# Kernel optimization log

Hardware: AMD Instinct MI355X
Metric: run time of the kernel (lower is better)

## Reference

```python
import jax, jax.numpy as jnp
import numpy as np

HID = 128  # args['hidden_size']


def preprocess_adj(A):
    # A: [B, N, N] -> D^{-1/2} (A + I) D^{-1/2}
    N = A.shape[1]
    A_hat = A + jnp.eye(N, dtype=A.dtype)
    d = jnp.sum(A_hat, axis=2)                     # [B, N]
    d_safe = jnp.where(d > 0, d, 1.0)
    d_inv = jnp.where(d > 0, d_safe ** -0.5, 0.0)  # inf -> 0, as in torch code
    return d_inv[:, :, None] * A_hat * d_inv[:, None, :]


def lstm(x, w_ih, w_hh, b_ih, b_hh):
    # x: [B, T, H]; PyTorch gate order i, f, g, o; zero init state
    B = x.shape[0]
    H = w_hh.shape[1]
    def step(carry, xt):
        h, c = carry
        z = xt @ w_ih.T + b_ih + h @ w_hh.T + b_hh
        i, f, g, o = jnp.split(z, 4, axis=-1)
        c = jax.nn.sigmoid(f) * c + jax.nn.sigmoid(i) * jnp.tanh(g)
        h = jax.nn.sigmoid(o) * jnp.tanh(c)
        return (h, c), h
    h0 = jnp.zeros((B, H), x.dtype)
    c0 = jnp.zeros((B, H), x.dtype)
    _, hs = jax.lax.scan(step, (h0, c0), jnp.swapaxes(x, 0, 1))
    return jnp.swapaxes(hs, 0, 1)  # [B, T, H]


def gcn_dynamic_forward(x, A_norm, conv_w, conv_b, w_ih, w_hh, b_ih, b_hh):
    # x: [B, N, HID] with N >= HID: take last HID rows as dynamic-filter input
    df_in = x[:, x.shape[1] - HID:, :]              # [B, HID, HID]
    dyn = jax.lax.conv_general_dilated(
        df_in, conv_w, window_strides=(1,), padding=[(1, 1)],
        dimension_numbers=('NCH', 'OIH', 'NCH')) + conv_b[None, :, None]
    lw = lstm(dyn, w_ih, w_hh, b_ih, b_hh)          # [B, HID, HID]
    agg = jnp.matmul(A_norm, x)                     # [B, N, HID]
    out = jax.nn.sigmoid(jnp.matmul(agg, lw))       # output activation (1-layer GCN)
    return out                                       # dropout is identity in eval


def setup_inputs() -> dict:
    key = jax.random.key(0)
    ks = jax.random.split(key, 8)
    B, N = 4, 4096
    node_embedding = jax.random.normal(ks[0], (B, N, HID), dtype=jnp.float32)
    # sparse symmetric-ish 0/1 adjacency, avg degree ~ N*0.01
    adjacency_matrix = (jax.random.uniform(ks[1], (B, N, N)) < 0.01).astype(jnp.float32)
    s = 0.05
    conv_w = jax.random.normal(ks[2], (HID, HID, 3), dtype=jnp.float32) * s
    conv_b = jax.random.normal(ks[3], (HID,), dtype=jnp.float32) * s
    w_ih = jax.random.normal(ks[4], (4 * HID, HID), dtype=jnp.float32) * s
    w_hh = jax.random.normal(ks[5], (4 * HID, HID), dtype=jnp.float32) * s
    b_ih = jax.random.normal(ks[6], (4 * HID,), dtype=jnp.float32) * s
    b_hh = jax.random.normal(ks[7], (4 * HID,), dtype=jnp.float32) * s
    return {"node_embedding": node_embedding, "adjacency_matrix": adjacency_matrix,
            "conv_w": conv_w, "conv_b": conv_b,
            "w_ih": w_ih, "w_hh": w_hh, "b_ih": b_ih, "b_hh": b_hh}


def reference(node_embedding, adjacency_matrix, conv_w, conv_b, w_ih, w_hh, b_ih, b_hh):
    A_norm = preprocess_adj(adjacency_matrix)
    return gcn_dynamic_forward(node_embedding, A_norm, conv_w, conv_b, w_ih, w_hh, b_ih, b_hh)
```

## Files before the change

kernel.cpp:

```cpp
#include <hip/hip_runtime.h>
#include <math.h>

#define N_NODES 4096
#define HIDN 128
#define MAXNZ 128

typedef float v4f __attribute__((ext_vector_type(4)));
typedef _Float16 h2 __attribute__((ext_vector_type(2)));
typedef _Float16 h8 __attribute__((ext_vector_type(8)));

__device__ __forceinline__ float fsig(float x) { return 1.0f / (1.0f + __expf(-x)); }
__device__ __forceinline__ float ftanh_(float x) { return 1.0f - 2.0f / (__expf(2.0f * x) + 1.0f); }

__global__ __launch_bounds__(512) void k_scan_conv(
        const float* __restrict__ A, float* __restrict__ d_inv,
        int* __restrict__ cnt, int* __restrict__ idx,
        const float* __restrict__ x, const float* __restrict__ conv_w,
        const float* __restrict__ conv_b, const float* __restrict__ w_ih,
        const float* __restrict__ b_ih, const float* __restrict__ b_hh,
        float* __restrict__ z4) {
    if (blockIdx.x < 2048) {
        const int wid = threadIdx.x >> 6;
        const int lane = threadIdx.x & 63;
        const int r = blockIdx.x * 8 + wid;
        const v4f* row = (const v4f*)(A + (size_t)r * N_NODES);
        __shared__ int sidx[8][MAXNZ];
        const unsigned long long below = (1ull << lane) - 1ull;
        int cbase = 0;
        v4f v[16];
        #pragma unroll
        for (int j = 0; j < 16; ++j)
            v[j] = row[j * 64 + lane];
#define PROC1(c, col)                                                         \
        {                                                                     \
            bool nz = ((c) != 0.0f);                                          \
            unsigned long long mm = __ballot(nz);                             \
            if (mm) {                                                         \
                if (nz) {                                                     \
                    int p_ = cbase + __popcll(mm & below);                    \
                    if (p_ < MAXNZ) sidx[wid][p_] = (col);                    \
                }                                                             \
                cbase += __popcll(mm);                                        \
            }                                                                 \
        }
        #pragma unroll
        for (int j = 0; j < 16; ++j) {
            int col0 = (j * 64 + lane) * 4;
            PROC1(v[j].x, col0 + 0);
            PROC1(v[j].y, col0 + 1);
            PROC1(v[j].z, col0 + 2);
            PROC1(v[j].w, col0 + 3);
        }
#undef PROC1
        int cnt_r = (cbase < MAXNZ) ? cbase : MAXNZ;
        for (int k = lane; k < cnt_r; k += 64)
            idx[r * MAXNZ + k] = sidx[wid][k];
        if (lane == 0) {
            cnt[r] = cnt_r;
            d_inv[r] = rsqrtf((float)(cbase + 1));
        }
    } else {
        const int cb = blockIdx.x - 2048;
        const int b = cb >> 5;
        const int t0 = (cb & 31) * 4;
        const int tsub = threadIdx.x >> 7;
        const int h = threadIdx.x & 127;
        const int t = t0 + tsub;
        __shared__ __align__(16) float dyn_lds[4][HIDN];
        const float* xb = x + ((size_t)b * N_NODES + (N_NODES - HIDN)) * HIDN;
        const float* w = conv_w + (size_t)t * HIDN * 3;
        float a0 = conv_b[t], a1 = 0.0f, a2 = 0.0f, a3 = 0.0f;
        #pragma unroll 4
        for (int i = 0; i < HIDN; i += 4) {
            const float* xr0 = xb + (size_t)i * HIDN;
            #pragma unroll
            for (int s = 0; s < 4; ++s) {
                const float* xr = xr0 + s * HIDN;
                float w0 = w[(i + s) * 3 + 0], w1 = w[(i + s) * 3 + 1], w2 = w[(i + s) * 3 + 2];
                float left  = (h > 0)   ? xr[h - 1] : 0.0f;
                float mid   = xr[h];
                float right = (h < 127) ? xr[h + 1] : 0.0f;
                if (s == 0)      a0 += left * w0 + mid * w1 + right * w2;
                else if (s == 1) a1 += left * w0 + mid * w1 + right * w2;
                else if (s == 2) a2 += left * w0 + mid * w1 + right * w2;
                else             a3 += left * w0 + mid * w1 + right * w2;
            }
        }
        dyn_lds[tsub][h] = (a0 + a1) + (a2 + a3);
        __syncthreads();
        const float4* dyn4 = (const float4*)dyn_lds[tsub];
        const int ch = t >> 4, si = t & 15;
        for (int qg = 0; qg < 4; ++qg) {
            int u = h + 128 * qg;
            const float4* wr = (const float4*)(w_ih + (size_t)u * HIDN);
            float za = b_ih[u] + b_hh[u];
            #pragma unroll
            for (int f4 = 0; f4 < 32; ++f4) {
                float4 wv = wr[f4];
                float4 dv = dyn4[f4];
                za += wv.x * dv.x + wv.y * dv.y + wv.z * dv.z + wv.w * dv.w;
            }
            z4[(((size_t)(b * 8 + ch) * 128 + h) * 4 + qg) * 16 + si] = za;
        }
    }
}

__global__ __launch_bounds__(512) void k_lstm_gather(
        const float* __restrict__ z4, const float* __restrict__ w_hh,
        float* __restrict__ lw,
        const float* __restrict__ x, const float* __restrict__ d_inv,
        const int* __restrict__ cnt, const int* __restrict__ idx,
        float* __restrict__ agg) {
    if (blockIdx.x < 4) {
        const int b = blockIdx.x;
        const int t = threadIdx.x;
        const int m = t >> 2;
        const int q = t & 3;
        __shared__ __align__(16) h2 hbuf[2][64];
        h2 w2[4][16];
        #pragma unroll
        for (int g = 0; g < 4; ++g) {
            const float4* wr = (const float4*)(w_hh + ((size_t)(g * HIDN + m)) * HIDN + q * 32);
            #pragma unroll
            for (int j4 = 0; j4 < 8; ++j4) {
                float4 wv = wr[j4];
                w2[g][2 * j4 + 0] = h2{(_Float16)wv.x, (_Float16)wv.y};
                w2[g][2 * j4 + 1] = h2{(_Float16)wv.z, (_Float16)wv.w};
            }
        }
        float c = 0.0f;
        if (t < 64) hbuf[0][t] = h2{(_Float16)0.0f, (_Float16)0.0f};
        __syncthreads();
        for (int ch = 0; ch < 8; ++ch) {
            const float4* zc = (const float4*)(z4 + ((((size_t)(b * 8 + ch) * 128 + m) * 4 + q) * 16));
            float4 zr0 = zc[0], zr1 = zc[1], zr2 = zc[2], zr3 = zc[3];
            float zs[16] = {zr0.x, zr0.y, zr0.z, zr0.w, zr1.x, zr1.y, zr1.z, zr1.w,
                            zr2.x, zr2.y, zr2.z, zr2.w, zr3.x, zr3.y, zr3.z, zr3.w};
            float hist[16];
            #pragma unroll
            for (int si = 0; si < 16; ++si) {
                const int s = ch * 16 + si;
                const h8* hq8 = ((const h8*)hbuf[s & 1]) + q * 4;
                h8 H0 = hq8[0], H1 = hq8[1], H2 = hq8[2], H3 = hq8[3];
                h2 hh[16];
                #pragma unroll
                for (int j = 0; j < 4; ++j) {
                    hh[j]      = ((const h2*)&H0)[j];
                    hh[4 + j]  = ((const h2*)&H1)[j];
                    hh[8 + j]  = ((const h2*)&H2)[j];
                    hh[12 + j] = ((const h2*)&H3)[j];
                }
                float zq = zs[si];
                float a0 = (q == 0) ? zq : 0.0f, b0 = 0.0f;
                float a1 = (q == 1) ? zq : 0.0f, b1 = 0.0f;
                float a2 = (q == 2) ? zq : 0.0f, b2 = 0.0f;
                float a3 = (q == 3) ? zq : 0.0f, b3 = 0.0f;
                #pragma unroll
                for (int j = 0; j < 8; ++j) {
                    a0 = __builtin_amdgcn_fdot2(w2[0][2 * j], hh[2 * j], a0, false);
                    b0 = __builtin_amdgcn_fdot2(w2[0][2 * j + 1], hh[2 * j + 1], b0, false);
                    a1 = __builtin_amdgcn_fdot2(w2[1][2 * j], hh[2 * j], a1, false);
                    b1 = __builtin_amdgcn_fdot2(w2[1][2 * j + 1], hh[2 * j + 1], b1, false);
                    a2 = __builtin_amdgcn_fdot2(w2[2][2 * j], hh[2 * j], a2, false);
                    b2 = __builtin_amdgcn_fdot2(w2[2][2 * j + 1], hh[2 * j + 1], b2, false);
                    a3 = __builtin_amdgcn_fdot2(w2[3][2 * j], hh[2 * j], a3, false);
                    b3 = __builtin_amdgcn_fdot2(w2[3][2 * j + 1], hh[2 * j + 1], b3, false);
                }
                float z0 = a0 + b0, z1 = a1 + b1, z2 = a2 + b2, z3 = a3 + b3;
                z0 += __shfl_xor(z0, 1); z0 += __shfl_xor(z0, 2);
                z1 += __shfl_xor(z1, 1); z1 += __shfl_xor(z1, 2);
                z2 += __shfl_xor(z2, 1); z2 += __shfl_xor(z2, 2);
                z3 += __shfl_xor(z3, 1); z3 += __shfl_xor(z3, 2);
                float ig = fsig(z0);
                float fg = fsig(z1);
                float gg = ftanh_(z2);
                float og = fsig(z3);
                c = fg * c + ig * gg;
                float hn = og * ftanh_(c);
                hist[si] = hn;
                if (q == 0) ((_Float16*)hbuf[(s + 1) & 1])[m] = (_Float16)hn;
                __syncthreads();
            }
            float* lwb = lw + ((size_t)b * HIDN + ch * 16) * HIDN + m;
            #pragma unroll
            for (int qq = 0; qq < 4; ++qq) {
                if (q == qq) {
                    #pragma unroll
                    for (int k = 0; k < 4; ++k)
                        lwb[(size_t)(qq * 4 + k) * HIDN] = hist[qq * 4 + k];
                }
            }
        }
    } else {
        const int gIdx = blockIdx.x - 4;
        const int b = (gIdx & 7) >> 1;
        const int o = ((gIdx >> 3) << 1) | (gIdx & 1);
        const int wid = threadIdx.x >> 6;
        const int lane = threadIdx.x & 63;
        __shared__ __align__(16) float dl[N_NODES];
        {
            const float4* dsrc = (const float4*)(d_inv + (b << 12));
            float4* ddst = (float4*)dl;
            ddst[threadIdx.x] = dsrc[threadIdx.x];
            ddst[threadIdx.x + 512] = dsrc[threadIdx.x + 512];
        }
        __syncthreads();
        const int i = o * 8 + wid;
        const int r = (b << 12) + i;
        const float2* xb = (const float2*)(x + (size_t)b * N_NODES * HIDN);
        const int* irow = idx + r * MAXNZ;
        const int n = cnt[r];
        float ax = 0.0f, ay = 0.0f;
        int k = 0;
        for (; k + 8 <= n; k += 8) {
            int4 j0 = *(const int4*)&irow[k];
            int4 j1 = *(const int4*)&irow[k + 4];
            float2 v0 = xb[(size_t)j0.x * 64 + lane];
            float2 v1 = xb[(size_t)j0.y * 64 + lane];
            float2 v2 = xb[(size_t)j0.z * 64 + lane];
            float2 v3 = xb[(size_t)j0.w * 64 + lane];
            float2 v4 = xb[(size_t)j1.x * 64 + lane];
            float2 v5 = xb[(size_t)j1.y * 64 + lane];
            float2 v6 = xb[(size_t)j1.z * 64 + lane];
            float2 v7 = xb[(size_t)j1.w * 64 + lane];
            float d0 = dl[j0.x], d1 = dl[j0.y], d2 = dl[j0.z], d3 = dl[j0.w];
            float d4 = dl[j1.x], d5 = dl[j1.y], d6 = dl[j1.z], d7 = dl[j1.w];
            ax += d0 * v0.x + d1 * v1.x + d2 * v2.x + d3 * v3.x
                + d4 * v4.x + d5 * v5.x + d6 * v6.x + d7 * v7.x;
            ay += d0 * v0.y + d1 * v1.y + d2 * v2.y + d3 * v3.y
                + d4 * v4.y + d5 * v5.y + d6 * v6.y + d7 * v7.y;
        }
        for (; k < n; ++k) {
            int j = irow[k];
            float dj = dl[j];
            float2 v = xb[(size_t)j * 64 + lane];
            ax += dj * v.x;
            ay += dj * v.y;
        }
        float di = dl[i];
        float2 vi = xb[(size_t)i * 64 + lane];
        float2 o2;
        o2.x = di * (ax + di * vi.x);
        o2.y = di * (ay + di * vi.y);
        ((float2*)(agg + (size_t)r * HIDN))[lane] = o2;
    }
}

__global__ __launch_bounds__(256) void k_outmm(
        const float* __restrict__ agg, const float* __restrict__ lw,
        float* __restrict__ out) {
    __shared__ __align__(16) float lw_lds[HIDN * HIDN];
    const int i0 = blockIdx.x * 64;
    const int b = i0 >> 12;
    const float4* lwg = (const float4*)(lw + (size_t)b * HIDN * HIDN);
    float4* lds4 = (float4*)lw_lds;
    for (int v = threadIdx.x; v < HIDN * HIDN / 4; v += 256) lds4[v] = lwg[v];
    __syncthreads();
    const int r0 = i0 + (threadIdx.x >> 3) * 2;
    const int u0 = (threadIdx.x & 7) * 16;
    const float4* a4 = (const float4*)agg;
    float4 acc[2][4];
    #pragma unroll
    for (int rr = 0; rr < 2; ++rr)
        #pragma unroll
        for (int cc = 0; cc < 4; ++cc) acc[rr][cc] = make_float4(0.f, 0.f, 0.f, 0.f);
    for (int f4 = 0; f4 < 32; ++f4) {
        float4 a0 = a4[(size_t)r0 * 32 + f4];
        float4 a1 = a4[(size_t)(r0 + 1) * 32 + f4];
        #pragma unroll
        for (int ff = 0; ff < 4; ++ff) {
            float af0 = (ff == 0) ? a0.x : (ff == 1) ? a0.y : (ff == 2) ? a0.z : a0.w;
            float af1 = (ff == 0) ? a1.x : (ff == 1) ? a1.y : (ff == 2) ? a1.z : a1.w;
            int f = f4 * 4 + ff;
            const float4* wrow = (const float4*)(lw_lds + f * HIDN + u0);
            #pragma unroll
            for (int cc = 0; cc < 4; ++cc) {
                float4 wv = wrow[cc];
                acc[0][cc].x += af0 * wv.x; acc[0][cc].y += af0 * wv.y;
                acc[0][cc].z += af0 * wv.z; acc[0][cc].w += af0 * wv.w;
                acc[1][cc].x += af1 * wv.x; acc[1][cc].y += af1 * wv.y;
                acc[1][cc].z += af1 * wv.z; acc[1][cc].w += af1 * wv.w;
            }
        }
    }
    #pragma unroll
    for (int rr = 0; rr < 2; ++rr) {
        #pragma unroll
        for (int cc = 0; cc < 4; ++cc) {
            float4 ov;
            ov.x = fsig(acc[rr][cc].x);
            ov.y = fsig(acc[rr][cc].y);
            ov.z = fsig(acc[rr][cc].z);
            ov.w = fsig(acc[rr][cc].w);
            *(float4*)(out + (size_t)(r0 + rr) * HIDN + u0 + cc * 4) = ov;
        }
    }
}

extern "C" void kernel_launch(void* const* d_in, const int* in_sizes, int n_in,
                              void* d_out, int out_size, void* d_ws, size_t ws_size,
                              hipStream_t stream) {
    const float* x      = (const float*)d_in[0];
    const float* A      = (const float*)d_in[1];
    const float* conv_w = (const float*)d_in[2];
    const float* conv_b = (const float*)d_in[3];
    const float* w_ih   = (const float*)d_in[4];
    const float* w_hh   = (const float*)d_in[5];
    const float* b_ih   = (const float*)d_in[6];
    const float* b_hh   = (const float*)d_in[7];
    float* out = (float*)d_out;

    char* ws = (char*)d_ws;
    float* d_inv = (float*)ws;
    int*   cnt   = (int*)(ws + 65536);
    int*   idx   = (int*)(ws + 131072);
    float* z4    = (float*)(ws + 131072 + 8388608);
    float* lw    = (float*)(ws + 131072 + 8388608 + 1048576);
    float* agg   = (float*)(ws + 131072 + 8388608 + 1048576 + 262144);

    hipLaunchKernelGGL(k_scan_conv, dim3(2176), dim3(512), 0, stream,
                       A, d_inv, cnt, idx,
                       x, conv_w, conv_b, w_ih, b_ih, b_hh, z4);
    hipLaunchKernelGGL(k_lstm_gather, dim3(2052), dim3(512), 0, stream,
                       z4, w_hh, lw, x, d_inv, cnt, idx, agg);
    hipLaunchKernelGGL(k_outmm, dim3(256), dim3(256), 0, stream, agg, lw, out);
}
```

Before: 562.5 us.

## Split fused scan/conv kernel and software-pipeline adjacency row scan

Splits the combined adjacency-scan and conv/input-projection kernel into two separate kernels. The conv kernel now has each thread compute one gate row across four timesteps, reusing each w_ih row for four dot products and writing the results as a float4. The scan kernel uses 256-thread blocks and double-buffers row loads in groups of four so the next loads are in flight while the ballot compaction runs. This cuts redundant w_ih reads and register pressure, at the cost of one extra kernel launch.

```diff
diff --git a/kernel.cpp b/kernel.cpp
--- a/kernel.cpp
+++ b/kernel.cpp
@@ -12,61 +12,19 @@
 __device__ __forceinline__ float fsig(float x) { return 1.0f / (1.0f + __expf(-x)); }
 __device__ __forceinline__ float ftanh_(float x) { return 1.0f - 2.0f / (__expf(2.0f * x) + 1.0f); }
 
-__global__ __launch_bounds__(512) void k_scan_conv(
-        const float* __restrict__ A, float* __restrict__ d_inv,
-        int* __restrict__ cnt, int* __restrict__ idx,
+__global__ __launch_bounds__(512) void k_convz(
         const float* __restrict__ x, const float* __restrict__ conv_w,
         const float* __restrict__ conv_b, const float* __restrict__ w_ih,
         const float* __restrict__ b_ih, const float* __restrict__ b_hh,
         float* __restrict__ z4) {
-    if (blockIdx.x < 2048) {
-        const int wid = threadIdx.x >> 6;
-        const int lane = threadIdx.x & 63;
-        const int r = blockIdx.x * 8 + wid;
-        const v4f* row = (const v4f*)(A + (size_t)r * N_NODES);
-        __shared__ int sidx[8][MAXNZ];
-        const unsigned long long below = (1ull << lane) - 1ull;
-        int cbase = 0;
-        v4f v[16];
-        #pragma unroll
-        for (int j = 0; j < 16; ++j)
-            v[j] = row[j * 64 + lane];
-#define PROC1(c, col)                                                         \
-        {                                                                     \
-            bool nz = ((c) != 0.0f);                                          \
-            unsigned long long mm = __ballot(nz);                             \
-            if (mm) {                                                         \
-                if (nz) {                                                     \
-                    int p_ = cbase + __popcll(mm & below);                    \
-                    if (p_ < MAXNZ) sidx[wid][p_] = (col);                    \
-                }                                                             \
-                cbase += __popcll(mm);                                        \
-            }                                                                 \
-        }
-        #pragma unroll
-        for (int j = 0; j < 16; ++j) {
-            int col0 = (j * 64 + lane) * 4;
-            PROC1(v[j].x, col0 + 0);
-            PROC1(v[j].y, col0 + 1);
-            PROC1(v[j].z, col0 + 2);
-            PROC1(v[j].w, col0 + 3);
-        }
-#undef PROC1
-        int cnt_r = (cbase < MAXNZ) ? cbase : MAXNZ;
-        for (int k = lane; k < cnt_r; k += 64)
-            idx[r * MAXNZ + k] = sidx[wid][k];
-        if (lane == 0) {
-            cnt[r] = cnt_r;
-            d_inv[r] = rsqrtf((float)(cbase + 1));
-        }
-    } else {
-        const int cb = blockIdx.x - 2048;
-        const int b = cb >> 5;
-        const int t0 = (cb & 31) * 4;
-        const int tsub = threadIdx.x >> 7;
-        const int h = threadIdx.x & 127;
-        const int t = t0 + tsub;
-        __shared__ __align__(16) float dyn_lds[4][HIDN];
+    const int cb = blockIdx.x;
+    const int b = cb >> 5;
+    const int t0 = (cb & 31) * 4;
+    const int tsub = threadIdx.x >> 7;
+    const int h = threadIdx.x & 127;
+    const int t = t0 + tsub;
+    __shared__ __align__(16) float dyn_lds[4][HIDN];
+    {
         const float* xb = x + ((size_t)b * N_NODES + (N_NODES - HIDN)) * HIDN;
         const float* w = conv_w + (size_t)t * HIDN * 3;
         float a0 = conv_b[t], a1 = 0.0f, a2 = 0.0f, a3 = 0.0f;
@@ -87,21 +45,87 @@
             }
         }
         dyn_lds[tsub][h] = (a0 + a1) + (a2 + a3);
-        __syncthreads();
-        const float4* dyn4 = (const float4*)dyn_lds[tsub];
-        const int ch = t >> 4, si = t & 15;
-        for (int qg = 0; qg < 4; ++qg) {
-            int u = h + 128 * qg;
-            const float4* wr = (const float4*)(w_ih + (size_t)u * HIDN);
-            float za = b_ih[u] + b_hh[u];
-            #pragma unroll
-            for (int f4 = 0; f4 < 32; ++f4) {
-                float4 wv = wr[f4];
-                float4 dv = dyn4[f4];
-                za += wv.x * dv.x + wv.y * dv.y + wv.z * dv.z + wv.w * dv.w;
-            }
-            z4[(((size_t)(b * 8 + ch) * 128 + h) * 4 + qg) * 16 + si] = za;
-        }
+    }
+    __syncthreads();
+    const int u = threadIdx.x;
+    const int qg = u >> 7;
+    const int m  = u & 127;
+    const float4* wr = (const float4*)(w_ih + (size_t)u * HIDN);
+    float bias = b_ih[u] + b_hh[u];
+    float acc0 = bias, acc1 = bias, acc2 = bias, acc3 = bias;
+    #pragma unroll
+    for (int half = 0; half < 2; ++half) {
+        float4 wv[16];
+        #pragma unroll
+        for (int j = 0; j < 16; ++j) wv[j] = wr[half * 16 + j];
+        const float4* d0 = (const float4*)dyn_lds[0] + half * 16;
+        const float4* d1 = (const float4*)dyn_lds[1] + half * 16;
+        const float4* d2 = (const float4*)dyn_lds[2] + half * 16;
+        const float4* d3 = (const float4*)dyn_lds[3] + half * 16;
+        #pragma unroll
+        for (int j = 0; j < 16; ++j) {
+            float4 wj = wv[j];
+            float4 v0 = d0[j], v1 = d1[j], v2 = d2[j], v3 = d3[j];
+            acc0 += wj.x * v0.x + wj.y * v0.y + wj.z * v0.z + wj.w * v0.w;
+            acc1 += wj.x * v1.x + wj.y * v1.y + wj.z * v1.z + wj.w * v1.w;
+            acc2 += wj.x * v2.x + wj.y * v2.y + wj.z * v2.z + wj.w * v2.w;
+            acc3 += wj.x * v3.x + wj.y * v3.y + wj.z * v3.z + wj.w * v3.w;
+        }
+    }
+    const int ch = t0 >> 4, si0 = t0 & 15;
+    float4 st = make_float4(acc0, acc1, acc2, acc3);
+    *(float4*)&z4[((((size_t)(b * 8 + ch)) * 128 + m) * 4 + qg) * 16 + si0] = st;
+}
+
+__global__ __launch_bounds__(256) void k_scan(
+        const float* __restrict__ A, float* __restrict__ d_inv,
+        int* __restrict__ cnt, int* __restrict__ idx) {
+    const int wid = threadIdx.x >> 6;
+    const int lane = threadIdx.x & 63;
+    const int r = blockIdx.x * 4 + wid;
+    const v4f* row = (const v4f*)(A + (size_t)r * N_NODES);
+    __shared__ int sidx[4][MAXNZ];
+    const unsigned long long below = (1ull << lane) - 1ull;
+    int cbase = 0;
+    v4f cur[4], nxt[4];
+    #pragma unroll
+    for (int j = 0; j < 4; ++j) cur[j] = row[j * 64 + lane];
+#define PROC1(c, col)                                                         \
+    {                                                                         \
+        bool nz = ((c) != 0.0f);                                              \
+        unsigned long long mm = __ballot(nz);                                 \
+        if (mm) {                                                             \
+            if (nz) {                                                         \
+                int p_ = cbase + __popcll(mm & below);                        \
+                if (p_ < MAXNZ) sidx[wid][p_] = (col);                        \
+            }                                                                 \
+            cbase += __popcll(mm);                                            \
+        }                                                                     \
+    }
+    #pragma unroll
+    for (int g = 0; g < 4; ++g) {
+        if (g < 3) {
+            #pragma unroll
+            for (int j = 0; j < 4; ++j) nxt[j] = row[(g + 1) * 256 + j * 64 + lane];
+        }
+        #pragma unroll
+        for (int j = 0; j < 4; ++j) {
+            int col0 = ((g * 4 + j) * 64 + lane) * 4;
+            PROC1(cur[j].x, col0 + 0);
+            PROC1(cur[j].y, col0 + 1);
+            PROC1(cur[j].z, col0 + 2);
+            PROC1(cur[j].w, col0 + 3);
+        }
+        #pragma unroll
+        for (int j = 0; j < 4; ++j) cur[j] = nxt[j];
+    }
+#undef PROC1
+    int cnt_r = (cbase < MAXNZ) ? cbase : MAXNZ;
+    for (int k = lane; k < cnt_r; k += 64)
+        idx[r * MAXNZ + k] = sidx[wid][k];
+    if (lane == 0) {
+        cnt[r] = cnt_r;
+        d_inv[r] = rsqrtf((float)(cbase + 1));
     }
 }
 
@@ -318,9 +342,10 @@
     float* lw    = (float*)(ws + 131072 + 8388608 + 1048576);
     float* agg   = (float*)(ws + 131072 + 8388608 + 1048576 + 262144);
 
-    hipLaunchKernelGGL(k_scan_conv, dim3(2176), dim3(512), 0, stream,
-                       A, d_inv, cnt, idx,
+    hipLaunchKernelGGL(k_convz, dim3(128), dim3(512), 0, stream,
                        x, conv_w, conv_b, w_ih, b_ih, b_hh, z4);
+    hipLaunchKernelGGL(k_scan, dim3(4096), dim3(256), 0, stream,
+                       A, d_inv, cnt, idx);
     hipLaunchKernelGGL(k_lstm_gather, dim3(2052), dim3(512), 0, stream,
                        z4, w_hh, lw, x, d_inv, cnt, idx, agg);
     hipLaunchKernelGGL(k_outmm, dim3(256), dim3(256), 0, stream, agg, lw, out);
```

New measurement: 528.8 us. 6.0% less time.
